# Optimization experiments

Measured on AMD Instinct MI355X. Metric: run time of the kernel, lower is better.

Reference implementation:

```python
import jax, jax.numpy as jnp
import numpy as np

H, D = 8, 16            # head_num, qkv_dim
E = H * D               # embedding_dim = 128
SQRT_E = float(np.sqrt(E))
LOGIT_CLIP = 10.0
MAX_DELTA = 4           # decoder_priority_bias_max_delta
TEMP = 0.8              # sampling_temperature
TOP_K = 20              # sampling_top_k


def setup_inputs() -> dict:
    key = jax.random.key(0)
    ks = jax.random.split(key, 12)
    B, P, N = 256, 200, 200
    s = 1.0 / np.sqrt(E)
    return {
        "encoded_nodes": jax.random.normal(ks[0], (B, N, E), jnp.float32),
        "encoded_first_node": jax.random.normal(ks[1], (B, P, E), jnp.float32),
        "encoded_last_node": jax.random.normal(ks[2], (B, P, E), jnp.float32),
        "ninf_mask": jnp.zeros((B, P, N), jnp.float32),
        "group_ids": jax.random.randint(ks[3], (B, N), 0, 5, jnp.int32),
        "current_min_priority": jax.random.randint(ks[4], (B, P), 0, 5, jnp.int32),
        "Wq_first": jax.random.normal(ks[5], (E, H * D), jnp.float32) * s,
        "Wq_last": jax.random.normal(ks[6], (E, H * D), jnp.float32) * s,
        "Wk": jax.random.normal(ks[7], (E, H * D), jnp.float32) * s,
        "Wv": jax.random.normal(ks[8], (E, H * D), jnp.float32) * s,
        "Wc": jax.random.normal(ks[9], (H * D, E), jnp.float32) * s,
        "bc": jax.random.normal(ks[10], (E,), jnp.float32) * 0.01,
        # learnable priority bias table: init * exp(-delta / tau)
        "bias_table": 0.2 * jnp.exp(-jnp.arange(MAX_DELTA + 1, dtype=jnp.float32)),
    }


def _heads(x):
    # [B, n, H*D] -> [B, H, n, D]
    B, n, _ = x.shape
    return x.reshape(B, n, H, D).transpose(0, 2, 1, 3)


def reference(encoded_nodes, encoded_first_node, encoded_last_node, ninf_mask,
              group_ids, current_min_priority,
              Wq_first, Wq_last, Wk, Wv, Wc, bc, bias_table):
    B, P, N = ninf_mask.shape
    # set_q1 + per-step q_last, q = q_first + q_last
    q = _heads(encoded_first_node @ Wq_first) + _heads(encoded_last_node @ Wq_last)
    k = _heads(encoded_nodes @ Wk)  # [B,H,N,D]
    v = _heads(encoded_nodes @ Wv)
    # masked multi-head attention with rank-3 ninf mask
    score = jnp.einsum('bhpd,bhnd->bhpn', q, k) / jnp.sqrt(jnp.float32(D))
    score = score + ninf_mask[:, None, :, :]
    w = jax.nn.softmax(score, axis=-1)
    out = jnp.einsum('bhpn,bhnd->bhpd', w, v)          # [B,H,P,D]
    out_concat = out.transpose(0, 2, 1, 3).reshape(B, P, H * D)
    mh = out_concat @ Wc + bc                          # multi_head_combine
    # single-head pointer attention
    sc = jnp.einsum('bpe,bne->bpn', mh, encoded_nodes)
    score_clipped = LOGIT_CLIP * jnp.tanh(sc / SQRT_E)
    # decoder priority bias (learnable table indexed by clamped delta)
    delta = jnp.clip(group_ids[:, None, :] - current_min_priority[:, :, None], 0, MAX_DELTA)
    pbias = bias_table[delta] * jnp.isfinite(ninf_mask)
    probs = jax.nn.softmax(score_clipped + pbias + ninf_mask, axis=-1)
    # sampling controls (eval): temperature then top-k filtering, renormalize
    adj = jnp.power(jnp.maximum(probs, 1e-12), 1.0 / TEMP)
    vals, idx = jax.lax.top_k(adj, TOP_K)
    bi = jnp.arange(B)[:, None, None]
    pi = jnp.arange(P)[None, :, None]
    filtered = jnp.zeros_like(adj).at[bi, pi, idx].set(vals)
    denom = jnp.maximum(filtered.sum(axis=-1, keepdims=True), 1e-12)
    return filtered / denom
```

## Files before the change

kernel.cpp:

```cpp
#include <hip/hip_runtime.h>
#include <hip/hip_bf16.h>
#include <math.h>

constexpr int B = 256, P = 200, N = 200, E = 128, H = 8, D = 16;
constexpr float INV_SQRT_D = 0.25f;
constexpr float INV_SQRT_E = 0.08838834764831845f;
constexpr float LOGIT_CLIP = 10.0f;
constexpr float INV_TEMP = 1.25f;
constexpr int TOP_K = 20;
constexpr int MAX_DELTA = 4;

__device__ __forceinline__ float dot4(float4 a, float4 b) {
    return a.x*b.x + a.y*b.y + a.z*b.z + a.w*b.w;
}

__global__ __launch_bounds__(256) void proj_kernel(
    const float* __restrict__ X1, const float* __restrict__ W1,
    const float* __restrict__ X2, const float* __restrict__ W2,
    const float* __restrict__ bias, float* __restrict__ out)
{
    __shared__ float4 xs[64][32];
    const int tid = threadIdx.x;
    const int eg = tid & 31;
    const int rg = tid >> 5;
    const int r0 = rg * 8;
    const long base = (long)blockIdx.x * 64;

    float acc[8][4];
    #pragma unroll
    for (int i = 0; i < 8; ++i)
        #pragma unroll
        for (int j = 0; j < 4; ++j) acc[i][j] = 0.f;

    for (int pass = 0; pass < 2; ++pass) {
        const float* X = pass ? X2 : X1;
        const float* W = pass ? W2 : W1;
        if (!X) break;
        if (pass) __syncthreads();
        const float4* X4 = (const float4*)X;
        for (int idx = tid; idx < 64 * 32; idx += 256) {
            int r = idx >> 5, c = idx & 31;
            xs[r][c] = X4[(base + r) * 32 + c];
        }
        __syncthreads();
        for (int c4 = 0; c4 < 32; ++c4) {
            float4 w0 = *(const float4*)&W[(c4*4+0)*128 + eg*4];
            float4 w1 = *(const float4*)&W[(c4*4+1)*128 + eg*4];
            float4 w2 = *(const float4*)&W[(c4*4+2)*128 + eg*4];
            float4 w3 = *(const float4*)&W[(c4*4+3)*128 + eg*4];
            #pragma unroll
            for (int i = 0; i < 8; ++i) {
                float4 xv = xs[r0 + i][c4];
                acc[i][0] += xv.x*w0.x + xv.y*w1.x + xv.z*w2.x + xv.w*w3.x;
                acc[i][1] += xv.x*w0.y + xv.y*w1.y + xv.z*w2.y + xv.w*w3.y;
                acc[i][2] += xv.x*w0.z + xv.y*w1.z + xv.z*w2.z + xv.w*w3.z;
                acc[i][3] += xv.x*w0.w + xv.y*w1.w + xv.z*w2.w + xv.w*w3.w;
            }
        }
    }

    float4 bv = make_float4(0.f, 0.f, 0.f, 0.f);
    if (bias) bv = *(const float4*)&bias[eg*4];
    float4* out4 = (float4*)out;
    #pragma unroll
    for (int i = 0; i < 8; ++i) {
        out4[(base + r0 + i) * 32 + eg] =
            make_float4(acc[i][0]+bv.x, acc[i][1]+bv.y, acc[i][2]+bv.z, acc[i][3]+bv.w);
    }
}

__global__ __launch_bounds__(256) void kv_proj_kernel(
    const float* __restrict__ X, const float* __restrict__ Wk,
    const float* __restrict__ Wv, float* __restrict__ outK,
    float* __restrict__ outV)
{
    __shared__ float4 xs[64][32];
    const int tid = threadIdx.x;
    const int eg = tid & 31;
    const int rg = tid >> 5;
    const int r0 = rg * 8;
    const long base = (long)blockIdx.x * 64;

    float acck[8][4], accv[8][4];
    #pragma unroll
    for (int i = 0; i < 8; ++i)
        #pragma unroll
        for (int j = 0; j < 4; ++j) { acck[i][j] = 0.f; accv[i][j] = 0.f; }

    const float4* X4 = (const float4*)X;
    for (int idx = tid; idx < 64 * 32; idx += 256) {
        int r = idx >> 5, c = idx & 31;
        xs[r][c] = X4[(base + r) * 32 + c];
    }
    __syncthreads();

    for (int c4 = 0; c4 < 32; ++c4) {
        float4 k0 = *(const float4*)&Wk[(c4*4+0)*128 + eg*4];
        float4 k1 = *(const float4*)&Wk[(c4*4+1)*128 + eg*4];
        float4 k2 = *(const float4*)&Wk[(c4*4+2)*128 + eg*4];
        float4 k3 = *(const float4*)&Wk[(c4*4+3)*128 + eg*4];
        float4 v0 = *(const float4*)&Wv[(c4*4+0)*128 + eg*4];
        float4 v1 = *(const float4*)&Wv[(c4*4+1)*128 + eg*4];
        float4 v2 = *(const float4*)&Wv[(c4*4+2)*128 + eg*4];
        float4 v3 = *(const float4*)&Wv[(c4*4+3)*128 + eg*4];
        #pragma unroll
        for (int i = 0; i < 8; ++i) {
            float4 xv = xs[r0 + i][c4];
            acck[i][0] += xv.x*k0.x + xv.y*k1.x + xv.z*k2.x + xv.w*k3.x;
            acck[i][1] += xv.x*k0.y + xv.y*k1.y + xv.z*k2.y + xv.w*k3.y;
            acck[i][2] += xv.x*k0.z + xv.y*k1.z + xv.z*k2.z + xv.w*k3.z;
            acck[i][3] += xv.x*k0.w + xv.y*k1.w + xv.z*k2.w + xv.w*k3.w;
            accv[i][0] += xv.x*v0.x + xv.y*v1.x + xv.z*v2.x + xv.w*v3.x;
            accv[i][1] += xv.x*v0.y + xv.y*v1.y + xv.z*v2.y + xv.w*v3.y;
            accv[i][2] += xv.x*v0.z + xv.y*v1.z + xv.z*v2.z + xv.w*v3.z;
            accv[i][3] += xv.x*v0.w + xv.y*v1.w + xv.z*v2.w + xv.w*v3.w;
        }
    }

    float4* outK4 = (float4*)outK;
    float4* outV4 = (float4*)outV;
    #pragma unroll
    for (int i = 0; i < 8; ++i) {
        outK4[(base + r0 + i) * 32 + eg] =
            make_float4(acck[i][0], acck[i][1], acck[i][2], acck[i][3]);
        outV4[(base + r0 + i) * 32 + eg] =
            make_float4(accv[i][0], accv[i][1], accv[i][2], accv[i][3]);
    }
}

__global__ __launch_bounds__(256) void attn_kernel(
    const float* __restrict__ q, const float* __restrict__ k,
    const float* __restrict__ v, const float* __restrict__ mask,
    float* __restrict__ out)
{
    __shared__ float4 ks[N][4];
    __shared__ float4 vs[N][4];
    __shared__ float red[4];
    const int raw = blockIdx.x;
    const int g = raw >> 6, rr6 = raw & 63;
    const int h = rr6 >> 3;
    const int b = g * 8 + (rr6 & 7);
    const int tid = threadIdx.x;

    const float4* k4 = (const float4*)k;
    const float4* v4 = (const float4*)v;
    for (int idx = tid; idx < N * 4; idx += 256) {
        int n = idx >> 2, c = idx & 3;
        size_t off = (size_t)(b * N + n) * 32 + h * 4 + c;
        ks[n][c] = k4[off];
        vs[n][c] = v4[off];
    }
    __syncthreads();

    float nrm = 0.f;
    if (tid < N) {
        float4 a0 = ks[tid][0], a1 = ks[tid][1], a2 = ks[tid][2], a3 = ks[tid][3];
        nrm = dot4(a0,a0) + dot4(a1,a1) + dot4(a2,a2) + dot4(a3,a3);
    }
    float wm = nrm;
    #pragma unroll
    for (int off = 32; off > 0; off >>= 1) wm = fmaxf(wm, __shfl_xor(wm, off));
    if ((tid & 63) == 0) red[tid >> 6] = wm;
    __syncthreads();
    const float kmax2 = fmaxf(fmaxf(red[0], red[1]), fmaxf(red[2], red[3]));

    const int p = tid;
    if (p >= P) return;

    const float4* qr = (const float4*)q + (size_t)(b * P + p) * 32 + h * 4;
    float4 q0 = qr[0], q1 = qr[1], q2 = qr[2], q3 = qr[3];
    q0.x*=INV_SQRT_D; q0.y*=INV_SQRT_D; q0.z*=INV_SQRT_D; q0.w*=INV_SQRT_D;
    q1.x*=INV_SQRT_D; q1.y*=INV_SQRT_D; q1.z*=INV_SQRT_D; q1.w*=INV_SQRT_D;
    q2.x*=INV_SQRT_D; q2.y*=INV_SQRT_D; q2.z*=INV_SQRT_D; q2.w*=INV_SQRT_D;
    q3.x*=INV_SQRT_D; q3.y*=INV_SQRT_D; q3.z*=INV_SQRT_D; q3.w*=INV_SQRT_D;
    const float qn2 = dot4(q0,q0) + dot4(q1,q1) + dot4(q2,q2) + dot4(q3,q3);
    const float M = sqrtf(qn2 * kmax2);

    const float4* m4 = (const float4*)(mask + (size_t)(b * P + p) * N);

    float l = 0.f;
    float o[16];
    #pragma unroll
    for (int d = 0; d < 16; ++d) o[d] = 0.f;

    #pragma unroll 2
    for (int n4 = 0; n4 < N / 4; ++n4) {
        float4 mv = m4[n4];
        float mvf[4] = {mv.x, mv.y, mv.z, mv.w};
        #pragma unroll
        for (int j = 0; j < 4; ++j) {
            int n = n4 * 4 + j;
            float s = dot4(q0, ks[n][0]) + dot4(q1, ks[n][1]) +
                      dot4(q2, ks[n][2]) + dot4(q3, ks[n][3]);
            float w = __expf(s + mvf[j] - M);
            l += w;
            float4 v0 = vs[n][0], v1 = vs[n][1], v2 = vs[n][2], v3 = vs[n][3];
            o[0]  += w*v0.x; o[1]  += w*v0.y; o[2]  += w*v0.z; o[3]  += w*v0.w;
            o[4]  += w*v1.x; o[5]  += w*v1.y; o[6]  += w*v1.z; o[7]  += w*v1.w;
            o[8]  += w*v2.x; o[9]  += w*v2.y; o[10] += w*v2.z; o[11] += w*v2.w;
            o[12] += w*v3.x; o[13] += w*v3.y; o[14] += w*v3.z; o[15] += w*v3.w;
        }
    }

    float inv_l = 1.f / l;
    float4* out4 = (float4*)out;
    size_t ob = (size_t)(b * P + p) * 32 + h * 4;
    #pragma unroll
    for (int c = 0; c < 4; ++c)
        out4[ob + c] = make_float4(o[c*4]*inv_l, o[c*4+1]*inv_l,
                                   o[c*4+2]*inv_l, o[c*4+3]*inv_l);
}

__global__ __launch_bounds__(256) void pointer_kernel(
    const float* __restrict__ mh, const float* __restrict__ nodes,
    const float* __restrict__ mask, const int* __restrict__ gid,
    const int* __restrict__ cmp, const float* __restrict__ btab,
    float* __restrict__ out)
{
    __shared__ float4 as[64][17];
    __shared__ float4 bs[64][17];
    const int b = blockIdx.z;
    const int p_base = blockIdx.y * 64;
    const int n_base = blockIdx.x * 64;
    const int tid = threadIdx.x;
    const int pi = tid >> 4;
    const int ni = tid & 15;

    const float4* mh4 = (const float4*)mh;
    const float4* nodes4 = (const float4*)nodes;

    float acc[4][4];
    #pragma unroll
    for (int i = 0; i < 4; ++i)
        #pragma unroll
        for (int j = 0; j < 4; ++j) acc[i][j] = 0.f;

    for (int ks = 0; ks < 2; ++ks) {
        if (ks) __syncthreads();
        #pragma unroll
        for (int t = 0; t < 4; ++t) {
            int idx = tid + 256 * t;
            int r = idx >> 4, c = idx & 15;
            int pr = p_base + r; pr = pr < P ? pr : P - 1;
            int nr = n_base + r; nr = nr < N ? nr : N - 1;
            as[r][c] = mh4[(size_t)(b * P + pr) * 32 + ks * 16 + c];
            bs[r][c] = nodes4[(size_t)(b * N + nr) * 32 + ks * 16 + c];
        }
        __syncthreads();

        for (int c4 = 0; c4 < 16; ++c4) {
            float4 a[4], w[4];
            #pragma unroll
            for (int i = 0; i < 4; ++i) a[i] = as[pi + 16 * i][c4];
            #pragma unroll
            for (int j = 0; j < 4; ++j) w[j] = bs[ni + 16 * j][c4];
            #pragma unroll
            for (int i = 0; i < 4; ++i)
                #pragma unroll
                for (int j = 0; j < 4; ++j)
                    acc[i][j] += dot4(a[i], w[j]);
        }
    }

    float bt[MAX_DELTA + 1];
    #pragma unroll
    for (int t = 0; t <= MAX_DELTA; ++t) bt[t] = btab[t];

    #pragma unroll
    for (int i = 0; i < 4; ++i) {
        int p = p_base + pi + 16 * i;
        if (p >= P) continue;
        int cm = cmp[b * P + p];
        #pragma unroll
        for (int j = 0; j < 4; ++j) {
            int n = n_base + ni + 16 * j;
            if (n >= N) continue;
            int g = gid[b * N + n];
            int delta = g - cm;
            delta = delta < 0 ? 0 : (delta > MAX_DELTA ? MAX_DELTA : delta);
            float mv = mask[(size_t)(b * P + p) * N + n];
            float pb = isfinite(mv) ? bt[delta] : 0.f;
            float logit = LOGIT_CLIP * tanhf(acc[i][j] * INV_SQRT_E) + pb + mv;
            out[(size_t)(b * P + p) * N + n] = logit;
        }
    }
}

__global__ __launch_bounds__(256) void topk_kernel(float* __restrict__ io)
{
    const int wv = threadIdx.x >> 6, lane = threadIdx.x & 63;
    const long row = (long)blockIdx.x * 4 + wv;
    float* r = io + row * N;

    float x[4];
    unsigned u[4];
    #pragma unroll
    for (int j = 0; j < 4; ++j) {
        int n = lane + 64 * j;
        bool valid = n < N;
        x[j] = valid ? r[n] : -INFINITY;
        unsigned bb = __float_as_uint(x[j]);
        u[j] = valid ? ((bb & 0x80000000u) ? ~bb : (bb | 0x80000000u)) : 0u;
    }

    unsigned p = 0;
    for (int i = 31; i >= 0; --i) {
        unsigned c = p | (1u << i);
        int cnt = 0;
        #pragma unroll
        for (int j = 0; j < 4; ++j)
            cnt += (int)__popcll(__ballot(u[j] >= c));
        if (cnt >= TOP_K) p = c;
    }

    int cnt_gt = 0;
    #pragma unroll
    for (int j = 0; j < 4; ++j)
        cnt_gt += (int)__popcll(__ballot(u[j] > p));
    const int needed = TOP_K - cnt_gt;

    const unsigned long long lt_mask = (1ull << lane) - 1ull;
    bool sel[4];
    int eq_before = 0;
    #pragma unroll
    for (int j = 0; j < 4; ++j) {
        unsigned long long em = __ballot(u[j] == p);
        int myrank = eq_before + (int)__popcll(em & lt_mask);
        sel[j] = (u[j] > p) || ((u[j] == p) && (myrank < needed));
        eq_before += (int)__popcll(em);
    }

    unsigned tb = (p & 0x80000000u) ? (p & 0x7FFFFFFFu) : ~p;
    float Tf = __uint_as_float(tb);

    float e[4];
    float sum = 0.f;
    if (isfinite(Tf)) {
        #pragma unroll
        for (int j = 0; j < 4; ++j) {
            e[j] = sel[j] ? __expf((x[j] - Tf) * INV_TEMP) : 0.f;
            sum += e[j];
        }
    } else {
        #pragma unroll
        for (int j = 0; j < 4; ++j) {
            e[j] = sel[j] ? 1.f : 0.f;
            sum += e[j];
        }
    }
    #pragma unroll
    for (int off = 32; off > 0; off >>= 1) sum += __shfl_xor(sum, off);
    float inv = 1.f / sum;
    #pragma unroll
    for (int j = 0; j < 4; ++j) {
        int n = lane + 64 * j;
        if (n < N) r[n] = e[j] * inv;
    }
}

extern "C" void kernel_launch(void* const* d_in, const int* in_sizes, int n_in,
                              void* d_out, int out_size, void* d_ws, size_t ws_size,
                              hipStream_t stream) {
    const float* nodes = (const float*)d_in[0];
    const float* first = (const float*)d_in[1];
    const float* last  = (const float*)d_in[2];
    const float* mask  = (const float*)d_in[3];
    const int*   gid   = (const int*)d_in[4];
    const int*   cmp   = (const int*)d_in[5];
    const float* Wqf   = (const float*)d_in[6];
    const float* Wql   = (const float*)d_in[7];
    const float* Wk    = (const float*)d_in[8];
    const float* Wv    = (const float*)d_in[9];
    const float* Wc    = (const float*)d_in[10];
    const float* bc    = (const float*)d_in[11];
    const float* btab  = (const float*)d_in[12];
    float* out = (float*)d_out;

    float* ws   = (float*)d_ws;
    const size_t SLOT = (size_t)B * P * E;
    float* qb  = ws;
    float* kb  = ws + SLOT;
    float* vb  = ws + 2 * SLOT;
    float* ao  = ws + 3 * SLOT;

    const int M = B * P;

    proj_kernel<<<M / 64, 256, 0, stream>>>(first, Wqf, last, Wql, nullptr, qb);
    kv_proj_kernel<<<M / 64, 256, 0, stream>>>(nodes, Wk, Wv, kb, vb);

    attn_kernel<<<B * H, 256, 0, stream>>>(qb, kb, vb, mask, ao);

    proj_kernel<<<M / 64, 256, 0, stream>>>(ao, Wc, nullptr, nullptr, bc, qb);

    dim3 pgrid((N + 63) / 64, (P + 63) / 64, B);
    pointer_kernel<<<pgrid, 256, 0, stream>>>(qb, nodes, mask, gid, cmp, btab, out);

    topk_kernel<<<(B * P) / 4, 256, 0, stream>>>(out);
}
```

Measured before the change: 610.4 us.

## Stage projection weights in double-buffered shared memory with smaller row tiles

The projection GEMM kernels now stage weight tiles of 16 input rows in shared memory. The next tile is prefetched into registers during compute and written to the alternate buffer, instead of every thread reading weights straight from global memory. Row tiles shrink from 64 to 32 rows per block, with rows interleaved across thread groups, which doubles the grid size. This is meant to cut redundant global weight traffic and raise occupancy. In exchange it adds a barrier per k-chunk and halves per-thread output reuse.

```diff
diff --git a/kernel.cpp b/kernel.cpp
--- a/kernel.cpp
+++ b/kernel.cpp
@@ -19,16 +19,16 @@
     const float* __restrict__ X2, const float* __restrict__ W2,
     const float* __restrict__ bias, float* __restrict__ out)
 {
-    __shared__ float4 xs[64][32];
+    __shared__ float4 xs[32][32];
+    __shared__ float4 ws[2][16][32];
     const int tid = threadIdx.x;
     const int eg = tid & 31;
     const int rg = tid >> 5;
-    const int r0 = rg * 8;
-    const long base = (long)blockIdx.x * 64;
-
-    float acc[8][4];
-    #pragma unroll
-    for (int i = 0; i < 8; ++i)
+    const long base = (long)blockIdx.x * 32;
+
+    float acc[4][4];
+    #pragma unroll
+    for (int i = 0; i < 4; ++i)
         #pragma unroll
         for (int j = 0; j < 4; ++j) acc[i][j] = 0.f;
 
@@ -38,33 +38,62 @@
         if (!X) break;
         if (pass) __syncthreads();
         const float4* X4 = (const float4*)X;
-        for (int idx = tid; idx < 64 * 32; idx += 256) {
+        const float4* W4 = (const float4*)W;
+        #pragma unroll
+        for (int t = 0; t < 4; ++t) {
+            int idx = tid + 256 * t;
             int r = idx >> 5, c = idx & 31;
             xs[r][c] = X4[(base + r) * 32 + c];
         }
+        #pragma unroll
+        for (int t = 0; t < 2; ++t) {
+            int idx = tid + 256 * t;
+            int r = idx >> 5, c = idx & 31;
+            ws[0][r][c] = W4[r * 32 + c];
+        }
         __syncthreads();
-        for (int c4 = 0; c4 < 32; ++c4) {
-            float4 w0 = *(const float4*)&W[(c4*4+0)*128 + eg*4];
-            float4 w1 = *(const float4*)&W[(c4*4+1)*128 + eg*4];
-            float4 w2 = *(const float4*)&W[(c4*4+2)*128 + eg*4];
-            float4 w3 = *(const float4*)&W[(c4*4+3)*128 + eg*4];
-            #pragma unroll
-            for (int i = 0; i < 8; ++i) {
-                float4 xv = xs[r0 + i][c4];
-                acc[i][0] += xv.x*w0.x + xv.y*w1.x + xv.z*w2.x + xv.w*w3.x;
-                acc[i][1] += xv.x*w0.y + xv.y*w1.y + xv.z*w2.y + xv.w*w3.y;
-                acc[i][2] += xv.x*w0.z + xv.y*w1.z + xv.z*w2.z + xv.w*w3.z;
-                acc[i][3] += xv.x*w0.w + xv.y*w1.w + xv.z*w2.w + xv.w*w3.w;
+
+        for (int kc = 0; kc < 8; ++kc) {
+            const int cur = kc & 1;
+            float4 pf0, pf1;
+            if (kc < 7) {
+                int i0 = tid, i1 = tid + 256;
+                pf0 = W4[((kc + 1) * 16 + (i0 >> 5)) * 32 + (i0 & 31)];
+                pf1 = W4[((kc + 1) * 16 + (i1 >> 5)) * 32 + (i1 & 31)];
             }
+            #pragma unroll
+            for (int k4 = 0; k4 < 4; ++k4) {
+                float4 xv[4];
+                #pragma unroll
+                for (int i = 0; i < 4; ++i)
+                    xv[i] = xs[rg + 8 * i][kc * 4 + k4];
+                float4 w0 = ws[cur][k4 * 4 + 0][eg];
+                float4 w1 = ws[cur][k4 * 4 + 1][eg];
+                float4 w2 = ws[cur][k4 * 4 + 2][eg];
+                float4 w3 = ws[cur][k4 * 4 + 3][eg];
+                #pragma unroll
+                for (int i = 0; i < 4; ++i) {
+                    acc[i][0] += xv[i].x*w0.x + xv[i].y*w1.x + xv[i].z*w2.x + xv[i].w*w3.x;
+                    acc[i][1] += xv[i].x*w0.y + xv[i].y*w1.y + xv[i].z*w2.y + xv[i].w*w3.y;
+                    acc[i][2] += xv[i].x*w0.z + xv[i].y*w1.z + xv[i].z*w2.z + xv[i].w*w3.z;
+                    acc[i][3] += xv[i].x*w0.w + xv[i].y*w1.w + xv[i].z*w2.w + xv[i].w*w3.w;
+                }
+            }
+            if (kc < 7) {
+                int i0 = tid, i1 = tid + 256;
+                ws[cur ^ 1][i0 >> 5][i0 & 31] = pf0;
+                ws[cur ^ 1][i1 >> 5][i1 & 31] = pf1;
+                __syncthreads();
+            }
         }
     }
 
     float4 bv = make_float4(0.f, 0.f, 0.f, 0.f);
-    if (bias) bv = *(const float4*)&bias[eg*4];
+    if (bias) bv = *(const float4*)&bias[eg * 4];
     float4* out4 = (float4*)out;
     #pragma unroll
-    for (int i = 0; i < 8; ++i) {
-        out4[(base + r0 + i) * 32 + eg] =
+    for (int i = 0; i < 4; ++i) {
+        out4[(base + rg + 8 * i) * 32 + eg] =
             make_float4(acc[i][0]+bv.x, acc[i][1]+bv.y, acc[i][2]+bv.z, acc[i][3]+bv.w);
     }
 }
@@ -74,56 +103,91 @@
     const float* __restrict__ Wv, float* __restrict__ outK,
     float* __restrict__ outV)
 {
-    __shared__ float4 xs[64][32];
+    __shared__ float4 xs[32][32];
+    __shared__ float4 wsk[2][16][32];
+    __shared__ float4 wsv[2][16][32];
     const int tid = threadIdx.x;
     const int eg = tid & 31;
     const int rg = tid >> 5;
-    const int r0 = rg * 8;
-    const long base = (long)blockIdx.x * 64;
-
-    float acck[8][4], accv[8][4];
-    #pragma unroll
-    for (int i = 0; i < 8; ++i)
+    const long base = (long)blockIdx.x * 32;
+
+    float acck[4][4], accv[4][4];
+    #pragma unroll
+    for (int i = 0; i < 4; ++i)
         #pragma unroll
         for (int j = 0; j < 4; ++j) { acck[i][j] = 0.f; accv[i][j] = 0.f; }
 
     const float4* X4 = (const float4*)X;
-    for (int idx = tid; idx < 64 * 32; idx += 256) {
+    const float4* Wk4 = (const float4*)Wk;
+    const float4* Wv4 = (const float4*)Wv;
+    #pragma unroll
+    for (int t = 0; t < 4; ++t) {
+        int idx = tid + 256 * t;
         int r = idx >> 5, c = idx & 31;
         xs[r][c] = X4[(base + r) * 32 + c];
     }
+    #pragma unroll
+    for (int t = 0; t < 2; ++t) {
+        int idx = tid + 256 * t;
+        int r = idx >> 5, c = idx & 31;
+        wsk[0][r][c] = Wk4[r * 32 + c];
+        wsv[0][r][c] = Wv4[r * 32 + c];
+    }
     __syncthreads();
 
-    for (int c4 = 0; c4 < 32; ++c4) {
-        float4 k0 = *(const float4*)&Wk[(c4*4+0)*128 + eg*4];
-        float4 k1 = *(const float4*)&Wk[(c4*4+1)*128 + eg*4];
-        float4 k2 = *(const float4*)&Wk[(c4*4+2)*128 + eg*4];
-        float4 k3 = *(const float4*)&Wk[(c4*4+3)*128 + eg*4];
-        float4 v0 = *(const float4*)&Wv[(c4*4+0)*128 + eg*4];
-        float4 v1 = *(const float4*)&Wv[(c4*4+1)*128 + eg*4];
-        float4 v2 = *(const float4*)&Wv[(c4*4+2)*128 + eg*4];
-        float4 v3 = *(const float4*)&Wv[(c4*4+3)*128 + eg*4];
-        #pragma unroll
-        for (int i = 0; i < 8; ++i) {
-            float4 xv = xs[r0 + i][c4];
-            acck[i][0] += xv.x*k0.x + xv.y*k1.x + xv.z*k2.x + xv.w*k3.x;
-            acck[i][1] += xv.x*k0.y + xv.y*k1.y + xv.z*k2.y + xv.w*k3.y;
-            acck[i][2] += xv.x*k0.z + xv.y*k1.z + xv.z*k2.z + xv.w*k3.z;
-            acck[i][3] += xv.x*k0.w + xv.y*k1.w + xv.z*k2.w + xv.w*k3.w;
-            accv[i][0] += xv.x*v0.x + xv.y*v1.x + xv.z*v2.x + xv.w*v3.x;
-            accv[i][1] += xv.x*v0.y + xv.y*v1.y + xv.z*v2.y + xv.w*v3.y;
-            accv[i][2] += xv.x*v0.z + xv.y*v1.z + xv.z*v2.z + xv.w*v3.z;
-            accv[i][3] += xv.x*v0.w + xv.y*v1.w + xv.z*v2.w + xv.w*v3.w;
+    for (int kc = 0; kc < 8; ++kc) {
+        const int cur = kc & 1;
+        float4 pk0, pk1, pv0, pv1;
+        if (kc < 7) {
+            int i0 = tid, i1 = tid + 256;
+            int a0 = ((kc + 1) * 16 + (i0 >> 5)) * 32 + (i0 & 31);
+            int a1 = ((kc + 1) * 16 + (i1 >> 5)) * 32 + (i1 & 31);
+            pk0 = Wk4[a0]; pk1 = Wk4[a1];
+            pv0 = Wv4[a0]; pv1 = Wv4[a1];
+        }
+        #pragma unroll
+        for (int k4 = 0; k4 < 4; ++k4) {
+            float4 xv[4];
+            #pragma unroll
+            for (int i = 0; i < 4; ++i)
+                xv[i] = xs[rg + 8 * i][kc * 4 + k4];
+            float4 k0 = wsk[cur][k4 * 4 + 0][eg];
+            float4 k1 = wsk[cur][k4 * 4 + 1][eg];
+            float4 k2 = wsk[cur][k4 * 4 + 2][eg];
+            float4 k3 = wsk[cur][k4 * 4 + 3][eg];
+            float4 v0 = wsv[cur][k4 * 4 + 0][eg];
+            float4 v1 = wsv[cur][k4 * 4 + 1][eg];
+            float4 v2 = wsv[cur][k4 * 4 + 2][eg];
+            float4 v3 = wsv[cur][k4 * 4 + 3][eg];
+            #pragma unroll
+            for (int i = 0; i < 4; ++i) {
+                acck[i][0] += xv[i].x*k0.x + xv[i].y*k1.x + xv[i].z*k2.x + xv[i].w*k3.x;
+                acck[i][1] += xv[i].x*k0.y + xv[i].y*k1.y + xv[i].z*k2.y + xv[i].w*k3.y;
+                acck[i][2] += xv[i].x*k0.z + xv[i].y*k1.z + xv[i].z*k2.z + xv[i].w*k3.z;
+                acck[i][3] += xv[i].x*k0.w + xv[i].y*k1.w + xv[i].z*k2.w + xv[i].w*k3.w;
+                accv[i][0] += xv[i].x*v0.x + xv[i].y*v1.x + xv[i].z*v2.x + xv[i].w*v3.x;
+                accv[i][1] += xv[i].x*v0.y + xv[i].y*v1.y + xv[i].z*v2.y + xv[i].w*v3.y;
+                accv[i][2] += xv[i].x*v0.z + xv[i].y*v1.z + xv[i].z*v2.z + xv[i].w*v3.z;
+                accv[i][3] += xv[i].x*v0.w + xv[i].y*v1.w + xv[i].z*v2.w + xv[i].w*v3.w;
+            }
+        }
+        if (kc < 7) {
+            int i0 = tid, i1 = tid + 256;
+            wsk[cur ^ 1][i0 >> 5][i0 & 31] = pk0;
+            wsk[cur ^ 1][i1 >> 5][i1 & 31] = pk1;
+            wsv[cur ^ 1][i0 >> 5][i0 & 31] = pv0;
+            wsv[cur ^ 1][i1 >> 5][i1 & 31] = pv1;
+            __syncthreads();
         }
     }
 
     float4* outK4 = (float4*)outK;
     float4* outV4 = (float4*)outV;
     #pragma unroll
-    for (int i = 0; i < 8; ++i) {
-        outK4[(base + r0 + i) * 32 + eg] =
+    for (int i = 0; i < 4; ++i) {
+        outK4[(base + rg + 8 * i) * 32 + eg] =
             make_float4(acck[i][0], acck[i][1], acck[i][2], acck[i][3]);
-        outV4[(base + r0 + i) * 32 + eg] =
+        outV4[(base + rg + 8 * i) * 32 + eg] =
             make_float4(accv[i][0], accv[i][1], accv[i][2], accv[i][3]);
     }
 }
@@ -385,12 +449,12 @@
 
     const int M = B * P;
 
-    proj_kernel<<<M / 64, 256, 0, stream>>>(first, Wqf, last, Wql, nullptr, qb);
-    kv_proj_kernel<<<M / 64, 256, 0, stream>>>(nodes, Wk, Wv, kb, vb);
+    proj_kernel<<<M / 32, 256, 0, stream>>>(first, Wqf, last, Wql, nullptr, qb);
+    kv_proj_kernel<<<M / 32, 256, 0, stream>>>(nodes, Wk, Wv, kb, vb);
 
     attn_kernel<<<B * H, 256, 0, stream>>>(qb, kb, vb, mask, ao);
 
-    proj_kernel<<<M / 64, 256, 0, stream>>>(ao, Wc, nullptr, nullptr, bc, qb);
+    proj_kernel<<<M / 32, 256, 0, stream>>>(ao, Wc, nullptr, nullptr, bc, qb);
 
     dim3 pgrid((N + 63) / 64, (P + 63) / 64, B);
     pointer_kernel<<<pgrid, 256, 0, stream>>>(qb, nodes, mask, gid, cmp, btab, out);
```

New measurement: 580.2 us. 4.9% less time.
